# Kernel tuning notes

Measured on AMD Instinct MI355X. Metric: run time of the kernel, lower is better.

Reference implementation:

```python
import jax, jax.numpy as jnp
import numpy as np

EPS = 1e-6

def _pixel_idx(loc_orig, H, W):
    # loc in [-1,1] -> nearest pixel, row-major flat index (matches 0.5*(loc+1)*[W,H]-0.5, round, clamp)
    xy = 0.5 * (loc_orig + 1.0) * jnp.array([W, H], dtype=loc_orig.dtype) - 0.5
    xy = jnp.round(xy).astype(jnp.int32)
    px = jnp.clip(xy[..., 0], 0, W - 1)
    py = jnp.clip(xy[..., 1], 0, H - 1)
    return py * W + px  # [B, N0]


def setup_inputs() -> dict:
    key = jax.random.key(0)
    ks = jax.random.split(key, 8)
    B, N, C = 4, 4096, 768
    H, W = 128, 128
    N0 = H * W
    x = jax.random.normal(ks[0], (B, N, C), dtype=jnp.float32)
    loc_orig = jax.random.uniform(ks[1], (B, N0, 2), minval=-1.0, maxval=1.0, dtype=jnp.float32)
    idx_agg = jax.random.randint(ks[2], (B, N0), 0, N, dtype=jnp.int32)
    agg_weight = jax.random.uniform(ks[3], (B, N0), dtype=jnp.float32)
    w_dw = jax.random.normal(ks[4], (C, 1, 3, 3), dtype=jnp.float32) * 0.1
    b_dw = jax.random.normal(ks[5], (C,), dtype=jnp.float32) * 0.1
    w_skip = jax.random.normal(ks[6], (C,), dtype=jnp.float32) * 0.1
    return {"x": x, "loc_orig": loc_orig, "idx_agg": idx_agg, "agg_weight": agg_weight,
            "H": H, "W": W, "w_dw": w_dw, "b_dw": b_dw, "w_skip": w_skip}


def reference(x, loc_orig, idx_agg, agg_weight, H, W, w_dw, b_dw, w_skip):
    B, N, C = x.shape
    N0 = loc_orig.shape[1]
    idx_hw = _pixel_idx(loc_orig, H, W)                      # [B, N0]
    boff = jnp.arange(B, dtype=jnp.int32)[:, None]
    seg_hw = (idx_hw + boff * (H * W)).reshape(-1)           # [B*N0] pixel segments
    seg_tok = (idx_agg.astype(jnp.int32) + boff * N).reshape(-1)  # [B*N0] token segments

    # token2map_agg_mat: scatter each orig position's token feature into its pixel, average by count
    feats = jnp.take_along_axis(x, idx_agg[..., None].astype(jnp.int32), axis=1).reshape(B * N0, C)
    sums = jax.ops.segment_sum(feats, seg_hw, num_segments=B * H * W)
    cnts = jax.ops.segment_sum(jnp.ones((B * N0,), x.dtype), seg_hw, num_segments=B * H * W)
    x_map = sums / (cnts + EPS)[:, None]
    x_map = x_map.reshape(B, H, W, C).transpose(0, 3, 1, 2)  # [B, C, H, W]

    # depthwise 3x3 conv (groups = C), padding 1, stride 1, with bias
    x_map = jax.lax.conv_general_dilated(
        x_map, w_dw, window_strides=(1, 1), padding=((1, 1), (1, 1)),
        dimension_numbers=("NCHW", "OIHW", "NCHW"), feature_group_count=C)
    x_map = x_map + b_dw[None, :, None, None]

    # map2token_agg_fast_nearest: weighted average of pixel feats per token
    pix = x_map.transpose(0, 2, 3, 1).reshape(B * H * W, C)[seg_hw]   # [B*N0, C]
    w = agg_weight.reshape(B * N0).astype(x.dtype)
    tok_sum = jax.ops.segment_sum(pix * w[:, None], seg_tok, num_segments=B * N)
    tok_w = jax.ops.segment_sum(w, seg_tok, num_segments=B * N)
    tok = (tok_sum / (tok_w + EPS)[:, None]).reshape(B, N, C)

    # grouped Conv1d(k=1, groups=C, bias=False) skip path == per-channel scale
    return tok + x * w_skip[None, None, :]
```

## Files before the change

kernel.cpp:

```cpp
#include <hip/hip_runtime.h>
#include <hip/hip_bf16.h>

#define BB 4
#define NN 4096
#define CC 768
#define HH 128
#define WW 128
#define N0 (HH * WW)
#define HW (HH * WW)
#define EPS 1e-6f
#define NSAMP (BB * N0)
#define NPIX  (BB * HW)
#define NTOK  (BB * NN)

#define TP 8
#define CSUB 128
#define TROWU 132
#define NTILE (HH / TP)
#define CONV_BLOCKS (BB * (CC / CSUB) * NTILE * NTILE)

#define XPB 8
#define TPB 4

__device__ inline float bf2f(ushort u) {
    unsigned v = ((unsigned)u) << 16;
    return __uint_as_float(v);
}
__device__ inline ushort f2bf(float f) {
    __hip_bfloat16 h = __float2bfloat16(f);
    return *reinterpret_cast<ushort*>(&h);
}
__device__ inline float4 us4_to_f4(ushort4 u) {
    float4 r;
    r.x = bf2f(u.x); r.y = bf2f(u.y); r.z = bf2f(u.z); r.w = bf2f(u.w);
    return r;
}

__global__ void k_idx(const float* __restrict__ loc,
                      const int* __restrict__ idx_agg,
                      int* __restrict__ idx_hw,
                      int* __restrict__ count_pix,
                      int* __restrict__ count_tok) {
    int i = blockIdx.x * blockDim.x + threadIdx.x;
    if (i >= NSAMP) return;
    float lx = loc[2 * i + 0];
    float ly = loc[2 * i + 1];
    float fx = 0.5f * (lx + 1.0f) * (float)WW - 0.5f;
    float fy = 0.5f * (ly + 1.0f) * (float)HH - 0.5f;
    int px = (int)rintf(fx);
    int py = (int)rintf(fy);
    px = min(max(px, 0), WW - 1);
    py = min(max(py, 0), HH - 1);
    int pix = py * WW + px;
    idx_hw[i] = pix;
    int b = i >> 14;
    atomicAdd(&count_pix[(b << 14) + pix], 1);
    atomicAdd(&count_tok[(b << 12) + idx_agg[i]], 1);
}

__global__ __launch_bounds__(1024) void k_scan(const int* __restrict__ cnt_pix,
                                               int* __restrict__ off_pix,
                                               const int* __restrict__ cnt_tok,
                                               int* __restrict__ off_tok) {
    __shared__ int wpart[16];
    __shared__ int run_sh;
    int bid = blockIdx.x;
    const int* cnt;
    int* off;
    int n, base, vbase;
    if (bid < 4) {
        cnt = cnt_pix; off = off_pix; n = HW;
        base = bid << 14; vbase = bid << 14;
    } else {
        cnt = cnt_tok; off = off_tok; n = NN;
        base = (bid - 4) << 12; vbase = (bid - 4) << 14;
    }
    int t = threadIdx.x;
    int lane = t & 63;
    int wid = t >> 6;
    if (t == 0) run_sh = 0;
    __syncthreads();
    for (int it = 0; it < n; it += 1024) {
        int idx = it + t;
        int v = (idx < n) ? cnt[base + idx] : 0;
        int s = v;
#pragma unroll
        for (int d = 1; d < 64; d <<= 1) {
            int u = __shfl_up(s, d, 64);
            if (lane >= d) s += u;
        }
        if (lane == 63) wpart[wid] = s;
        __syncthreads();
        if (wid == 0) {
            int p = (lane < 16) ? wpart[lane] : 0;
#pragma unroll
            for (int d = 1; d < 16; d <<= 1) {
                int u = __shfl_up(p, d, 64);
                if (lane >= d) p += u;
            }
            if (lane < 16) wpart[lane] = p;
        }
        __syncthreads();
        int wbase = (wid == 0) ? 0 : wpart[wid - 1];
        int run = run_sh;
        if (idx < n) off[base + idx] = vbase + run + wbase + s - v;
        __syncthreads();
        if (t == 0) run_sh = run + wpart[15];
        __syncthreads();
    }
}

__global__ void k_fill(const int* __restrict__ idx_hw,
                       const int* __restrict__ idx_agg,
                       const int* __restrict__ off_pix, int* __restrict__ fill_pix,
                       int* __restrict__ list_pix,
                       const int* __restrict__ off_tok, int* __restrict__ fill_tok,
                       int* __restrict__ list_tok) {
    int i = blockIdx.x * blockDim.x + threadIdx.x;
    if (i >= NSAMP) return;
    int b = i >> 14;
    int sp = (b << 14) + idx_hw[i];
    int p = atomicAdd(&fill_pix[sp], 1);
    list_pix[off_pix[sp] + p] = i;
    int st = (b << 12) + idx_agg[i];
    int q = atomicAdd(&fill_tok[st], 1);
    list_tok[off_tok[st] + q] = i;
}

__global__ __launch_bounds__(192) void k_xmap(const float* __restrict__ x,
                                              const int* __restrict__ idx_agg,
                                              const int* __restrict__ count_pix,
                                              const int* __restrict__ off_pix,
                                              const int* __restrict__ list_pix,
                                              ushort* __restrict__ xm) {
    int bi0 = blockIdx.x * XPB;
    int b = bi0 >> 14;
    int c4 = threadIdx.x;
    const float* xb = x + (size_t)(b * NN) * CC;

    int kk[XPB], st[XPB];
#pragma unroll
    for (int p = 0; p < XPB; ++p) {
        kk[p] = count_pix[bi0 + p];
        st[p] = off_pix[bi0 + p];
    }
    float4 acc[XPB];
#pragma unroll
    for (int p = 0; p < XPB; ++p) acc[p] = make_float4(0.f, 0.f, 0.f, 0.f);

    int kmax = 0;
#pragma unroll
    for (int p = 0; p < XPB; ++p) kmax = max(kmax, kk[p]);

    for (int j = 0; j < kmax; ++j) {
#pragma unroll
        for (int p = 0; p < XPB; ++p) {
            if (j < kk[p]) {
                int i = list_pix[st[p] + j];
                int tok = idx_agg[i];
                float4 v = ((const float4*)(xb + (size_t)tok * CC))[c4];
                acc[p].x += v.x; acc[p].y += v.y;
                acc[p].z += v.z; acc[p].w += v.w;
            }
        }
    }
#pragma unroll
    for (int p = 0; p < XPB; ++p) {
        float inv = 1.0f / ((float)kk[p] + EPS);
        ushort4 o;
        o.x = f2bf(acc[p].x * inv); o.y = f2bf(acc[p].y * inv);
        o.z = f2bf(acc[p].z * inv); o.w = f2bf(acc[p].w * inv);
        ((ushort4*)(xm + (size_t)(bi0 + p) * CC))[c4] = o;
    }
}

__global__ __launch_bounds__(256, 4) void k_conv(const ushort* __restrict__ xm,
                                                 const int* __restrict__ count_pix,
                                                 const float* __restrict__ w_dw,
                                                 const float* __restrict__ b_dw,
                                                 ushort* __restrict__ ym) {
    __shared__ ushort tile[(TP + 2) * (TP + 2) * TROWU];
    __shared__ int cnt_tile[TP * TP];

    int f = blockIdx.x;
    f = (f & 7) * (CONV_BLOCKS / 8) + (f >> 3);
    int tx = f & 15;
    int ty = (f >> 4) & 15;
    int cblk = (f >> 8) % 6;
    int b = f / 1536;
    int tid = threadIdx.x;

    int c0g = cblk * CSUB;
    const ushort* src = xm + (size_t)(b << 14) * CC + c0g;

    if (tid < TP * TP) {
        int r = tid >> 3;
        int c = tid & 7;
        cnt_tile[tid] = count_pix[(b << 14) + (ty * TP + r) * WW + tx * TP + c];
    }
    for (int idx = tid; idx < (TP + 2) * (TP + 2) * (CSUB / 4); idx += 256) {
        int lc = idx & 31;
        int cell = idx >> 5;
        int r = cell / (TP + 2);
        int c = cell % (TP + 2);
        int gy = ty * TP + r - 1;
        int gx = tx * TP + c - 1;
        ushort4 v = {0, 0, 0, 0};
        if (gy >= 0 && gy < HH && gx >= 0 && gx < WW) {
            v = ((const ushort4*)(src + (size_t)(gy * WW + gx) * CC))[lc];
        }
        ((ushort4*)(tile + (size_t)cell * TROWU))[lc] = v;
    }
    __syncthreads();

    int c4 = tid & 31;
    int px = tid >> 5;

    int cnts[TP];
#pragma unroll
    for (int oy = 0; oy < TP; ++oy) cnts[oy] = cnt_tile[oy * TP + px];

    float wreg[36];
    {
        const float4* wp = (const float4*)(w_dw + (size_t)(c0g + c4 * 4) * 9);
#pragma unroll
        for (int j = 0; j < 9; ++j) ((float4*)wreg)[j] = wp[j];
    }
    float4 bias = ((const float4*)(b_dw + c0g))[c4];

    float4 a[3][3];
#pragma unroll
    for (int i = 0; i < 2; ++i)
#pragma unroll
        for (int j = 0; j < 3; ++j)
            a[i][j] = us4_to_f4(((const ushort4*)(tile + (size_t)(i * (TP + 2) + px + j) * TROWU))[c4]);

    ushort* dst_base = ym + (size_t)((b << 14) + (ty * TP) * WW + tx * TP + px) * CC
                       + c0g;

#pragma unroll
    for (int oy = 0; oy < TP; ++oy) {
#pragma unroll
        for (int j = 0; j < 3; ++j)
            a[2][j] = us4_to_f4(((const ushort4*)(tile + (size_t)((oy + 2) * (TP + 2) + px + j) * TROWU))[c4]);

        if (cnts[oy] > 0) {
            float4 acc = bias;
#pragma unroll
            for (int i = 0; i < 3; ++i) {
#pragma unroll
                for (int j = 0; j < 3; ++j) {
                    int t = i * 3 + j;
                    acc.x += a[i][j].x * wreg[0 * 9 + t];
                    acc.y += a[i][j].y * wreg[1 * 9 + t];
                    acc.z += a[i][j].z * wreg[2 * 9 + t];
                    acc.w += a[i][j].w * wreg[3 * 9 + t];
                }
            }
            ushort4 o;
            o.x = f2bf(acc.x); o.y = f2bf(acc.y); o.z = f2bf(acc.z); o.w = f2bf(acc.w);
            ((ushort4*)(dst_base + (size_t)oy * WW * CC))[c4] = o;
        }

#pragma unroll
        for (int j = 0; j < 3; ++j) {
            a[0][j] = a[1][j];
            a[1][j] = a[2][j];
        }
    }
}

__global__ __launch_bounds__(192) void k_token(const ushort* __restrict__ ym,
                                               const float* __restrict__ x,
                                               const float* __restrict__ agg_w,
                                               const int* __restrict__ idx_hw,
                                               const int* __restrict__ count_tok,
                                               const int* __restrict__ off_tok,
                                               const int* __restrict__ list_tok,
                                               const float* __restrict__ w_skip,
                                               float* __restrict__ out) {
    int bi0 = blockIdx.x * TPB;
    int b = bi0 >> 12;
    int c4 = threadIdx.x;
    const ushort* yb = ym + (size_t)(b << 14) * CC;

    int kk[TPB], st[TPB];
#pragma unroll
    for (int p = 0; p < TPB; ++p) {
        kk[p] = count_tok[bi0 + p];
        st[p] = off_tok[bi0 + p];
    }
    float4 acc[TPB];
    float tw[TPB];
#pragma unroll
    for (int p = 0; p < TPB; ++p) {
        acc[p] = make_float4(0.f, 0.f, 0.f, 0.f);
        tw[p] = 0.f;
    }

    int kmax = max(max(kk[0], kk[1]), max(kk[2], kk[3]));
    for (int j = 0; j < kmax; ++j) {
#pragma unroll
        for (int p = 0; p < TPB; ++p) {
            if (j < kk[p]) {
                int i = list_tok[st[p] + j];
                float w = agg_w[i];
                int pix = idx_hw[i];
                float4 v = us4_to_f4(((const ushort4*)(yb + (size_t)pix * CC))[c4]);
                acc[p].x += w * v.x; acc[p].y += w * v.y;
                acc[p].z += w * v.z; acc[p].w += w * v.w;
                tw[p] += w;
            }
        }
    }

    float4 ws = ((const float4*)w_skip)[c4];
#pragma unroll
    for (int p = 0; p < TPB; ++p) {
        float inv = 1.0f / (tw[p] + EPS);
        float4 xv = ((const float4*)(x + (size_t)(bi0 + p) * CC))[c4];
        float4 o;
        o.x = acc[p].x * inv + xv.x * ws.x;
        o.y = acc[p].y * inv + xv.y * ws.y;
        o.z = acc[p].z * inv + xv.z * ws.z;
        o.w = acc[p].w * inv + xv.w * ws.w;
        ((float4*)(out + (size_t)(bi0 + p) * CC))[c4] = o;
    }
}

extern "C" void kernel_launch(void* const* d_in, const int* in_sizes, int n_in,
                              void* d_out, int out_size, void* d_ws, size_t ws_size,
                              hipStream_t stream) {
    const float* x       = (const float*)d_in[0];
    const float* loc     = (const float*)d_in[1];
    const int*   idx_agg = (const int*)d_in[2];
    const float* agg_w   = (const float*)d_in[3];
    const float* w_dw    = (const float*)d_in[6];
    const float* b_dw    = (const float*)d_in[7];
    const float* w_skip  = (const float*)d_in[8];
    float* out = (float*)d_out;
    char* ws = (char*)d_ws;

    size_t off = 0;
    int* count_pix = (int*)(ws + off); off += (size_t)NPIX * 4;
    int* fill_pix  = (int*)(ws + off); off += (size_t)NPIX * 4;
    int* count_tok = (int*)(ws + off); off += (size_t)NTOK * 4;
    int* fill_tok  = (int*)(ws + off); off += (size_t)NTOK * 4;
    size_t zero_bytes = off;
    int* idx_hw   = (int*)(ws + off); off += (size_t)NSAMP * 4;
    int* off_pix  = (int*)(ws + off); off += (size_t)NPIX * 4;
    int* list_pix = (int*)(ws + off); off += (size_t)NSAMP * 4;
    int* off_tok  = (int*)(ws + off); off += (size_t)NTOK * 4;
    int* list_tok = (int*)(ws + off); off += (size_t)NSAMP * 4;
    ushort* xm = (ushort*)(ws + off); off += (size_t)NPIX * CC * 2;
    ushort* ym = (ushort*)(ws + off); off += (size_t)NPIX * CC * 2;

    hipMemsetAsync(ws, 0, zero_bytes, stream);

    hipLaunchKernelGGL(k_idx, dim3(NSAMP / 256), dim3(256), 0, stream,
                       loc, idx_agg, idx_hw, count_pix, count_tok);
    hipLaunchKernelGGL(k_scan, dim3(8), dim3(1024), 0, stream,
                       count_pix, off_pix, count_tok, off_tok);
    hipLaunchKernelGGL(k_fill, dim3(NSAMP / 256), dim3(256), 0, stream,
                       idx_hw, idx_agg, off_pix, fill_pix, list_pix,
                       off_tok, fill_tok, list_tok);
    hipLaunchKernelGGL(k_xmap, dim3(NPIX / XPB), dim3(192), 0, stream,
                       x, idx_agg, count_pix, off_pix, list_pix, xm);
    hipLaunchKernelGGL(k_conv, dim3(CONV_BLOCKS), dim3(256), 0, stream,
                       xm, count_pix, w_dw, b_dw, ym);
    hipLaunchKernelGGL(k_token, dim3(NTOK / TPB), dim3(192), 0, stream,
                       ym, x, agg_w, idx_hw, count_tok, off_tok, list_tok,
                       w_skip, out);
}
```

Before: 172.8 us.

## Skip empty-pixel stores and halo loads in conv; widen token gather batch

```diff
diff --git a/kernel.cpp b/kernel.cpp
--- a/kernel.cpp
+++ b/kernel.cpp
@@ -20,7 +20,7 @@
 #define CONV_BLOCKS (BB * (CC / CSUB) * NTILE * NTILE)
 
 #define XPB 8
-#define TPB 4
+#define TPB 8
 
 __device__ inline float bf2f(ushort u) {
     unsigned v = ((unsigned)u) << 16;
@@ -166,11 +166,13 @@
     }
 #pragma unroll
     for (int p = 0; p < XPB; ++p) {
-        float inv = 1.0f / ((float)kk[p] + EPS);
-        ushort4 o;
-        o.x = f2bf(acc[p].x * inv); o.y = f2bf(acc[p].y * inv);
-        o.z = f2bf(acc[p].z * inv); o.w = f2bf(acc[p].w * inv);
-        ((ushort4*)(xm + (size_t)(bi0 + p) * CC))[c4] = o;
+        if (kk[p] > 0) {
+            float inv = 1.0f / ((float)kk[p] + EPS);
+            ushort4 o;
+            o.x = f2bf(acc[p].x * inv); o.y = f2bf(acc[p].y * inv);
+            o.z = f2bf(acc[p].z * inv); o.w = f2bf(acc[p].w * inv);
+            ((ushort4*)(xm + (size_t)(bi0 + p) * CC))[c4] = o;
+        }
     }
 }
 
@@ -180,7 +182,7 @@
                                                  const float* __restrict__ b_dw,
                                                  ushort* __restrict__ ym) {
     __shared__ ushort tile[(TP + 2) * (TP + 2) * TROWU];
-    __shared__ int cnt_tile[TP * TP];
+    __shared__ int cnt_halo[(TP + 2) * (TP + 2)];
 
     int f = blockIdx.x;
     f = (f & 7) * (CONV_BLOCKS / 8) + (f >> 3);
@@ -193,32 +195,38 @@
     int c0g = cblk * CSUB;
     const ushort* src = xm + (size_t)(b << 14) * CC + c0g;
 
-    if (tid < TP * TP) {
-        int r = tid >> 3;
-        int c = tid & 7;
-        cnt_tile[tid] = count_pix[(b << 14) + (ty * TP + r) * WW + tx * TP + c];
-    }
-    for (int idx = tid; idx < (TP + 2) * (TP + 2) * (CSUB / 4); idx += 256) {
-        int lc = idx & 31;
-        int cell = idx >> 5;
-        int r = cell / (TP + 2);
-        int c = cell % (TP + 2);
+    if (tid < (TP + 2) * (TP + 2)) {
+        int r = tid / 10;
+        int c = tid - r * 10;
         int gy = ty * TP + r - 1;
         int gx = tx * TP + c - 1;
-        ushort4 v = {0, 0, 0, 0};
-        if (gy >= 0 && gy < HH && gx >= 0 && gx < WW) {
-            v = ((const ushort4*)(src + (size_t)(gy * WW + gx) * CC))[lc];
-        }
-        ((ushort4*)(tile + (size_t)cell * TROWU))[lc] = v;
+        int cnt = 0;
+        if (gy >= 0 && gy < HH && gx >= 0 && gx < WW)
+            cnt = count_pix[(b << 14) + gy * WW + gx];
+        cnt_halo[tid] = cnt;
+    }
+    __syncthreads();
+
+    {
+        int lc = tid & 31;
+        int cell = tid >> 5;
+        int r = 0, c = cell;
+        int gy = ty * TP - 1;
+        int gx = tx * TP - 1 + c;
+        for (; cell < (TP + 2) * (TP + 2); cell += 8) {
+            ushort4 v = {0, 0, 0, 0};
+            if (cnt_halo[cell] > 0) {
+                v = ((const ushort4*)(src + (size_t)(gy * WW + gx) * CC))[lc];
+            }
+            ((ushort4*)(tile + (size_t)cell * TROWU))[lc] = v;
+            c += 8; gx += 8;
+            if (c >= (TP + 2)) { c -= (TP + 2); gx -= (TP + 2); r += 1; gy += 1; }
+        }
     }
     __syncthreads();
 
     int c4 = tid & 31;
     int px = tid >> 5;
-
-    int cnts[TP];
-#pragma unroll
-    for (int oy = 0; oy < TP; ++oy) cnts[oy] = cnt_tile[oy * TP + px];
 
     float wreg[36];
     {
@@ -244,7 +252,7 @@
         for (int j = 0; j < 3; ++j)
             a[2][j] = us4_to_f4(((const ushort4*)(tile + (size_t)((oy + 2) * (TP + 2) + px + j) * TROWU))[c4]);
 
-        if (cnts[oy] > 0) {
+        if (cnt_halo[(oy + 1) * (TP + 2) + px + 1] > 0) {
             float4 acc = bias;
 #pragma unroll
             for (int i = 0; i < 3; ++i) {
@@ -298,7 +306,10 @@
         tw[p] = 0.f;
     }
 
-    int kmax = max(max(kk[0], kk[1]), max(kk[2], kk[3]));
+    int kmax = 0;
+#pragma unroll
+    for (int p = 0; p < TPB; ++p) kmax = max(kmax, kk[p]);
+
     for (int j = 0; j < kmax; ++j) {
 #pragma unroll
         for (int p = 0; p < TPB; ++p) {
```

After: 168.3 us. 2.6% less time.
